# Kernel tuning notes

Measured on AMD Instinct MI355X. Metric: run time of the kernel, lower is better.

Reference implementation:

```python
import jax, jax.numpy as jnp
import numpy as np

N, E, D = 100000, 1600000, 128
EPS = 1e-5
NUM_LAYERS = 5


def setup_inputs() -> dict:
    key = jax.random.key(0)
    ks = jax.random.split(key, 2 + 2 * NUM_LAYERS)
    inp = {
        "x": jax.random.normal(ks[0], (N, D), dtype=jnp.float32),
        "edge_index": jax.random.randint(ks[1], (2, E), 0, N),
    }
    for i in range(NUM_LAYERS):
        inp[f"W{i}"] = jax.random.normal(ks[2 + 2 * i], (D, D), dtype=jnp.float32) / np.sqrt(D).astype(np.float32)
        inp[f"b{i}"] = jax.random.normal(ks[3 + 2 * i], (D,), dtype=jnp.float32) * 0.01
    return inp


def _gcn_forward(x, edge_index, Ws, bs):
    src, dst = edge_index[0], edge_index[1]
    # Degree with self-loops (torch code appends arange(N) loops, then clamps
    # count at min=1; with loops deg >= 1 always, so clamp is a no-op).
    deg = jax.ops.segment_sum(jnp.ones((E,), x.dtype), dst, num_segments=N) + 1.0
    inv_deg = (1.0 / deg)[:, None]  # [N, 1]
    for W, b in zip(Ws, bs):
        h = x @ W.T  # [N, D] linear (no bias; bias added after aggregation)
        # mean aggregation over in-neighbors + self-loop message (= h itself)
        agg = (jax.ops.segment_sum(h[src], dst, num_segments=N) + h) * inv_deg + b
        # batch_norm in training mode, no affine, biased variance, eps=1e-5
        mean = agg.mean(axis=0)
        var = ((agg - mean) ** 2).mean(axis=0)
        x = jax.nn.relu((agg - mean) * jax.lax.rsqrt(var + EPS))
        # dropout p=0.0, eval mode -> identity
    return x


def reference(x, edge_index, W0, b0, W1, b1, W2, b2, W3, b3, W4, b4):
    return _gcn_forward(x, edge_index, (W0, W1, W2, W3, W4), (b0, b1, b2, b3, b4))
```

## Files before the change

### kernel.cpp

```cpp
#include <hip/hip_runtime.h>
#include <hip/hip_bf16.h>

#define DD 128
#define NPART 8

typedef __bf16 bf16x8 __attribute__((ext_vector_type(8)));
typedef float f32x4 __attribute__((ext_vector_type(4)));

__device__ inline unsigned short f2bf_rne(float f) {
    unsigned u = __float_as_uint(f);
    u += 0x7fff + ((u >> 16) & 1);
    return (unsigned short)(u >> 16);
}


__global__ __launch_bounds__(256) void hist_kernel(const int* __restrict__ dst,
                                                   int* __restrict__ cnt, int E, int psize) {
    int part = blockIdx.x & (NPART - 1);
    int lo = part * psize, hi = lo + psize;
    int stride = (gridDim.x >> 3) * 256;
    for (int e = (blockIdx.x >> 3) * 256 + threadIdx.x; e < E; e += stride) {
        int d = dst[e];
        if (d >= lo && d < hi) atomicAdd(&cnt[d], 1);
    }
}

__global__ void scanA_kernel(const int* __restrict__ cnt, int* __restrict__ row_off,
                             int* __restrict__ partials, int N) {
    __shared__ int ls[256];
    int tid = threadIdx.x;
    int i = blockIdx.x * 1024 + tid * 4;
    int c0 = (i + 0 < N) ? cnt[i + 0] : 0;
    int c1 = (i + 1 < N) ? cnt[i + 1] : 0;
    int c2 = (i + 2 < N) ? cnt[i + 2] : 0;
    int c3 = (i + 3 < N) ? cnt[i + 3] : 0;
    int tot = c0 + c1 + c2 + c3;
    ls[tid] = tot;
    __syncthreads();
    for (int off = 1; off < 256; off <<= 1) {
        int v = (tid >= off) ? ls[tid - off] : 0;
        __syncthreads();
        ls[tid] += v;
        __syncthreads();
    }
    int excl = ls[tid] - tot;
    if (tid == 255) partials[blockIdx.x] = ls[255];
    int e0 = excl, e1 = e0 + c0, e2 = e1 + c1, e3 = e2 + c2;
    if (i + 0 < N) row_off[i + 0] = e0;
    if (i + 1 < N) row_off[i + 1] = e1;
    if (i + 2 < N) row_off[i + 2] = e2;
    if (i + 3 < N) row_off[i + 3] = e3;
}

__global__ __launch_bounds__(256) void scanB_kernel(int* partials, int nb) {
    __shared__ int ls[256];
    int tid = threadIdx.x;
    int base = 0;
    for (int c = 0; c < nb; c += 256) {
        int v = (c + tid < nb) ? partials[c + tid] : 0;
        ls[tid] = v;
        __syncthreads();
        for (int off = 1; off < 256; off <<= 1) {
            int t = (tid >= off) ? ls[tid - off] : 0;
            __syncthreads();
            ls[tid] += t;
            __syncthreads();
        }
        if (c + tid < nb) partials[c + tid] = ls[tid] - v + base;
        int tot = ls[255];
        __syncthreads();
        base += tot;
    }
}

__global__ void scanC_kernel(const int* __restrict__ cnt, int* __restrict__ row_off,
                             int* __restrict__ cursor, float* __restrict__ inv_deg,
                             const int* __restrict__ partials, int N) {
    int tid = threadIdx.x;
    int i = blockIdx.x * 1024 + tid * 4;
    int add = partials[blockIdx.x];
#pragma unroll
    for (int m = 0; m < 4; m++) {
        int idx = i + m;
        if (idx < N) {
            int v = row_off[idx] + add;
            row_off[idx] = v;
            cursor[idx] = v;
            int c = cnt[idx];
            inv_deg[idx] = 1.0f / (float)(c + 1);
            if (idx == N - 1) row_off[N] = v + c;
        }
    }
}

__global__ __launch_bounds__(256) void scatter_kernel(const int* __restrict__ src,
                                                      const int* __restrict__ dst,
                                                      int* __restrict__ cursor,
                                                      int* __restrict__ csr, int E, int psize) {
    int part = blockIdx.x & (NPART - 1);
    int lo = part * psize, hi = lo + psize;
    int stride = (gridDim.x >> 3) * 256;
    for (int e = (blockIdx.x >> 3) * 256 + threadIdx.x; e < E; e += stride) {
        int d = dst[e];
        if (d >= lo && d < hi) {
            int pos = atomicAdd(&cursor[d], 1);
            csr[pos] = src[e];
        }
    }
}


__global__ __launch_bounds__(256) void tobf16_kernel(const float* __restrict__ x,
                                                     unsigned short* __restrict__ h, long total4) {
    long idx = (long)blockIdx.x * 256 + threadIdx.x;
    if (idx >= total4) return;
    float4 v = ((const float4*)x)[idx];
    ushort4 o;
    o.x = f2bf_rne(v.x); o.y = f2bf_rne(v.y); o.z = f2bf_rne(v.z); o.w = f2bf_rne(v.w);
    ((ushort4*)h)[idx] = o;
}


template <int NORM>
__global__ __launch_bounds__(256) void gather_kernel(const unsigned int* __restrict__ prev,
                                                     const int* __restrict__ row_off,
                                                     const int* __restrict__ csr,
                                                     const float* __restrict__ stats,
                                                     float* __restrict__ sbuf, int N) {
    int node = blockIdx.x * 4 + (threadIdx.x >> 6);
    if (node >= N) return;
    int lane = threadIdx.x & 63;
    float m0 = 0.f, m1 = 0.f, r0 = 1.f, r1 = 1.f;
    if (NORM) {
        int c = 2 * lane;
        m0 = stats[c];       m1 = stats[c + 1];
        r0 = stats[128 + c]; r1 = stats[129 + c];
    }
    int base = node * 64 + lane;
    float ax, ay;
    {
        unsigned u = prev[base];
        float vx = __uint_as_float(u << 16);
        float vy = __uint_as_float(u & 0xffff0000u);
        if (NORM) { ax = fmaxf((vx - m0) * r0, 0.f); ay = fmaxf((vy - m1) * r1, 0.f); }
        else      { ax = vx; ay = vy; }
    }
    int e = row_off[node], end = row_off[node + 1];
    for (; e + 4 <= end; e += 4) {
        int i0 = csr[e], i1 = csr[e + 1], i2 = csr[e + 2], i3 = csr[e + 3];
        unsigned u0 = prev[i0 * 64 + lane];
        unsigned u1 = prev[i1 * 64 + lane];
        unsigned u2 = prev[i2 * 64 + lane];
        unsigned u3 = prev[i3 * 64 + lane];
        float x0 = __uint_as_float(u0 << 16), y0 = __uint_as_float(u0 & 0xffff0000u);
        float x1 = __uint_as_float(u1 << 16), y1 = __uint_as_float(u1 & 0xffff0000u);
        float x2 = __uint_as_float(u2 << 16), y2 = __uint_as_float(u2 & 0xffff0000u);
        float x3 = __uint_as_float(u3 << 16), y3 = __uint_as_float(u3 & 0xffff0000u);
        if (NORM) {
            ax += fmaxf((x0 - m0) * r0, 0.f) + fmaxf((x1 - m0) * r0, 0.f)
                + fmaxf((x2 - m0) * r0, 0.f) + fmaxf((x3 - m0) * r0, 0.f);
            ay += fmaxf((y0 - m1) * r1, 0.f) + fmaxf((y1 - m1) * r1, 0.f)
                + fmaxf((y2 - m1) * r1, 0.f) + fmaxf((y3 - m1) * r1, 0.f);
        } else {
            ax += x0 + x1 + x2 + x3;
            ay += y0 + y1 + y2 + y3;
        }
    }
    for (; e < end; e++) {
        unsigned u0 = prev[csr[e] * 64 + lane];
        float x0 = __uint_as_float(u0 << 16), y0 = __uint_as_float(u0 & 0xffff0000u);
        if (NORM) { ax += fmaxf((x0 - m0) * r0, 0.f); ay += fmaxf((y0 - m1) * r1, 0.f); }
        else      { ax += x0; ay += y0; }
    }
    float2 o; o.x = ax; o.y = ay;
    ((float2*)sbuf)[base] = o;
}


__global__ void wsplit_kernel(const float* __restrict__ W0, const float* __restrict__ W1,
                              const float* __restrict__ W2, const float* __restrict__ W3,
                              const float* __restrict__ W4, unsigned short* __restrict__ whl) {
    int idx = blockIdx.x * 256 + threadIdx.x;
    int l = idx >> 14, r = idx & 16383;
    const float* W = (l == 0) ? W0 : (l == 1) ? W1 : (l == 2) ? W2 : (l == 3) ? W3 : W4;
    float x = W[r];
    unsigned u = __float_as_uint(x);
    unsigned short h = (unsigned short)(u >> 16);
    float hf = __uint_as_float(u & 0xffff0000u);
    float lo = x - hf;
    unsigned short lw = (unsigned short)(__float_as_uint(lo) >> 16);
    whl[l * 32768 + r] = h;
    whl[l * 32768 + 16384 + r] = lw;
}


template <int LAST>
__global__ __launch_bounds__(256) void mgemm_kernel(const float* __restrict__ Sin,
                                                    unsigned short* __restrict__ outh,
                                                    float* __restrict__ Sio,
                                                    const unsigned short* __restrict__ Whl,
                                                    const float* __restrict__ bias,
                                                    const float* __restrict__ inv_deg,
                                                    float* __restrict__ stats, int N) {
    __shared__ unsigned short ShL[128 * 128];
    __shared__ unsigned short SlL[128 * 128];
    const int t = threadIdx.x;
    const int i0 = blockIdx.x * 128;

#pragma unroll
    for (int b = 0; b < 16; b++) {
        int f = t + 256 * b;
        int r = f >> 5, k4 = f & 31;
        int row = i0 + r;
        float4 v = (row < N) ? *(const float4*)&Sin[(size_t)row * 128 + k4 * 4]
                             : make_float4(0.f, 0.f, 0.f, 0.f);
        int k8 = k4 >> 1;
        int base = r * 128 + ((k8 ^ (r & 7)) * 8) + (k4 & 1) * 4;
        ushort4 h, lw;
        {
            unsigned u = __float_as_uint(v.x); h.x = (unsigned short)(u >> 16);
            float d = v.x - __uint_as_float(u & 0xffff0000u); lw.x = (unsigned short)(__float_as_uint(d) >> 16);
            u = __float_as_uint(v.y); h.y = (unsigned short)(u >> 16);
            d = v.y - __uint_as_float(u & 0xffff0000u); lw.y = (unsigned short)(__float_as_uint(d) >> 16);
            u = __float_as_uint(v.z); h.z = (unsigned short)(u >> 16);
            d = v.z - __uint_as_float(u & 0xffff0000u); lw.z = (unsigned short)(__float_as_uint(d) >> 16);
            u = __float_as_uint(v.w); h.w = (unsigned short)(u >> 16);
            d = v.w - __uint_as_float(u & 0xffff0000u); lw.w = (unsigned short)(__float_as_uint(d) >> 16);
        }
        *(ushort4*)(ShL + base) = h;
        *(ushort4*)(SlL + base) = lw;
    }
    __syncthreads();

    const int w = t >> 6, l = t & 63;
    const int ll = l & 15, lh = l >> 4;
    const unsigned short* Wh = Whl;
    const unsigned short* Wl2 = Whl + 16384;
    f32x4 acc[2][8];
#pragma unroll
    for (int st = 0; st < 2; st++)
#pragma unroll
        for (int jt = 0; jt < 8; jt++) acc[st][jt] = (f32x4){0.f, 0.f, 0.f, 0.f};

    const int r0 = w * 32 + ll;
    const int r1 = r0 + 16;
#pragma unroll
    for (int ks = 0; ks < 4; ks++) {
        int k8 = ks * 4 + lh;
        int ia0 = r0 * 128 + ((k8 ^ (r0 & 7)) * 8);
        int ia1 = r1 * 128 + ((k8 ^ (r1 & 7)) * 8);
        bf16x8 ah0 = *(const bf16x8*)(ShL + ia0);
        bf16x8 al0 = *(const bf16x8*)(SlL + ia0);
        bf16x8 ah1 = *(const bf16x8*)(ShL + ia1);
        bf16x8 al1 = *(const bf16x8*)(SlL + ia1);
        int wk = ks * 32 + lh * 8;
#pragma unroll
        for (int jt = 0; jt < 8; jt++) {
            int wrow = jt * 16 + ll;
            bf16x8 bh = *(const bf16x8*)(Wh + wrow * 128 + wk);
            bf16x8 bl = *(const bf16x8*)(Wl2 + wrow * 128 + wk);
            acc[0][jt] = __builtin_amdgcn_mfma_f32_16x16x32_bf16(ah0, bh, acc[0][jt], 0, 0, 0);
            acc[1][jt] = __builtin_amdgcn_mfma_f32_16x16x32_bf16(ah1, bh, acc[1][jt], 0, 0, 0);
            acc[0][jt] = __builtin_amdgcn_mfma_f32_16x16x32_bf16(al0, bh, acc[0][jt], 0, 0, 0);
            acc[1][jt] = __builtin_amdgcn_mfma_f32_16x16x32_bf16(al1, bh, acc[1][jt], 0, 0, 0);
            acc[0][jt] = __builtin_amdgcn_mfma_f32_16x16x32_bf16(ah0, bl, acc[0][jt], 0, 0, 0);
            acc[1][jt] = __builtin_amdgcn_mfma_f32_16x16x32_bf16(ah1, bl, acc[1][jt], 0, 0, 0);
        }
    }

    float bj[8];
#pragma unroll
    for (int jt = 0; jt < 8; jt++) bj[jt] = bias[jt * 16 + ll];
    float cs[8], cq[8];
#pragma unroll
    for (int jt = 0; jt < 8; jt++) { cs[jt] = 0.f; cq[jt] = 0.f; }
#pragma unroll
    for (int st = 0; st < 2; st++) {
#pragma unroll
        for (int reg = 0; reg < 4; reg++) {
            int row = i0 + w * 32 + st * 16 + lh * 4 + reg;
            bool valid = row < N;
            float sc = valid ? inv_deg[row] : 0.f;
#pragma unroll
            for (int jt = 0; jt < 8; jt++) {
                float o = acc[st][jt][reg] * sc + bj[jt];
                if (valid) {
                    if (LAST) Sio[(size_t)row * 128 + jt * 16 + ll] = o;
                    else      outh[(size_t)row * 128 + jt * 16 + ll] = f2bf_rne(o);
                    cs[jt] += o;
                    cq[jt] += o * o;
                }
            }
        }
    }
#pragma unroll
    for (int jt = 0; jt < 8; jt++) {
        cs[jt] += __shfl_xor(cs[jt], 16);
        cs[jt] += __shfl_xor(cs[jt], 32);
        cq[jt] += __shfl_xor(cq[jt], 16);
        cq[jt] += __shfl_xor(cq[jt], 32);
    }
    __syncthreads();
    float* sred = (float*)ShL;
    if (l < 16) {
#pragma unroll
        for (int jt = 0; jt < 8; jt++) {
            sred[w * 256 + jt * 16 + l] = cs[jt];
            sred[w * 256 + 128 + jt * 16 + l] = cq[jt];
        }
    }
    __syncthreads();
    {
        int col = t & 127, s = t >> 7;
        float v = sred[0 * 256 + s * 128 + col] + sred[1 * 256 + s * 128 + col]
                + sred[2 * 256 + s * 128 + col] + sred[3 * 256 + s * 128 + col];
        atomicAdd(&stats[s * 128 + col], v);
    }
}


__global__ void finalize_kernel(float* stats, float invN) {
    int c = threadIdx.x;
    float mean = stats[c] * invN;
    float var = stats[128 + c] * invN - mean * mean;
    stats[c] = mean;
    stats[128 + c] = rsqrtf(var + 1e-5f);
}


__global__ __launch_bounds__(256) void outnorm_kernel(const float* __restrict__ agg,
                                                      const float* __restrict__ stats,
                                                      float* __restrict__ out, long total4) {
    long idx = (long)blockIdx.x * 256 + threadIdx.x;
    if (idx >= total4) return;
    int c0 = (int)((idx & 31) * 4);
    float4 v = ((const float4*)agg)[idx];
    float4 o;
    o.x = fmaxf((v.x - stats[c0 + 0]) * stats[128 + c0 + 0], 0.f);
    o.y = fmaxf((v.y - stats[c0 + 1]) * stats[128 + c0 + 1], 0.f);
    o.z = fmaxf((v.z - stats[c0 + 2]) * stats[128 + c0 + 2], 0.f);
    o.w = fmaxf((v.w - stats[c0 + 3]) * stats[128 + c0 + 3], 0.f);
    ((float4*)out)[idx] = o;
}


extern "C" void kernel_launch(void* const* d_in, const int* in_sizes, int n_in,
                              void* d_out, int out_size, void* d_ws, size_t ws_size,
                              hipStream_t stream) {
    const float* x = (const float*)d_in[0];
    const int* ei = (const int*)d_in[1];
    int N = in_sizes[0] / DD;
    int E = in_sizes[1] / 2;
    const float* Wp[5];
    const float* bp[5];
    for (int l = 0; l < 5; l++) {
        Wp[l] = (const float*)d_in[2 + 2 * l];
        bp[l] = (const float*)d_in[3 + 2 * l];
    }

    char* ws = (char*)d_ws;
    size_t off = 0;
    auto alloc = [&](size_t bytes) -> char* {
        char* p = ws + off;
        off = (off + bytes + 511) & ~(size_t)511;
        return p;
    };
    int* cnt = (int*)alloc((size_t)N * 4);
    int* row_off = (int*)alloc(((size_t)N + 1) * 4);
    int* cursor = (int*)alloc((size_t)N * 4);
    int* partials = (int*)alloc(4096 * 4);
    float* inv_deg = (float*)alloc((size_t)N * 4);
    float* stats = (float*)alloc(5 * 256 * 4);
    unsigned short* whl = (unsigned short*)alloc(5 * 32768 * 2);
    int* csr = (int*)alloc((size_t)E * 4);
    unsigned short* hb = (unsigned short*)alloc((size_t)N * DD * 2);
    float* Sbuf = (float*)alloc((size_t)N * DD * 4);
    (void)ws_size;

    const int* srcv = ei;
    const int* dstv = ei + E;

    hipMemsetAsync(cnt, 0, (size_t)N * 4, stream);
    hipMemsetAsync(stats, 0, 5 * 256 * 4, stream);

    wsplit_kernel<<<5 * 16384 / 256, 256, 0, stream>>>(Wp[0], Wp[1], Wp[2], Wp[3], Wp[4], whl);

    long total4 = (long)N * (DD / 4);
    tobf16_kernel<<<(int)((total4 + 255) / 256), 256, 0, stream>>>(x, hb, total4);

    int psize = (N + NPART - 1) / NPART;
    hist_kernel<<<NPART * 128, 256, 0, stream>>>(dstv, cnt, E, psize);
    int nb = (N + 1023) / 1024;
    scanA_kernel<<<nb, 256, 0, stream>>>(cnt, row_off, partials, N);
    scanB_kernel<<<1, 256, 0, stream>>>(partials, nb);
    scanC_kernel<<<nb, 256, 0, stream>>>(cnt, row_off, cursor, inv_deg, partials, N);
    scatter_kernel<<<NPART * 128, 256, 0, stream>>>(srcv, dstv, cursor, csr, E, psize);

    float invN = 1.0f / (float)N;
    int gblocks = (N + 3) / 4;
    int mblocks = (N + 127) / 128;

    for (int l = 0; l < 5; l++) {
        if (l == 0) {
            gather_kernel<0><<<gblocks, 256, 0, stream>>>((const unsigned int*)hb, row_off, csr,
                                                          nullptr, Sbuf, N);
        } else {
            gather_kernel<1><<<gblocks, 256, 0, stream>>>((const unsigned int*)hb, row_off, csr,
                                                          stats + (l - 1) * 256, Sbuf, N);
        }
        if (l < 4) {
            mgemm_kernel<0><<<mblocks, 256, 0, stream>>>(Sbuf, hb, nullptr, whl + l * 32768,
                                                         bp[l], inv_deg, stats + l * 256, N);
        } else {
            mgemm_kernel<1><<<mblocks, 256, 0, stream>>>(Sbuf, nullptr, Sbuf, whl + l * 32768,
                                                         bp[l], inv_deg, stats + l * 256, N);
        }
        finalize_kernel<<<1, 128, 0, stream>>>(stats + l * 256, invN);
    }

    outnorm_kernel<<<(int)((total4 + 255) / 256), 256, 0, stream>>>(Sbuf, stats + 4 * 256,
                                                                    (float*)d_out, total4);
}
```

Measured before the change: 1.015 ms.

## Store aggregated features in bf16, drop low-part MFMA, fold finalize into consumers

The gather now writes its aggregate as packed bf16 instead of fp32. The GEMM therefore loads half the bytes and skips the low-part activation split along with its two MFMAs per tile. The finalize kernel is removed: gather and outnorm compute mean and rsqrt from the raw sums themselves. The last layer also writes bf16 and outnorm reads it back, the gather loop is unrolled to 8, and the histogram and scatter grids are doubled. These changes cut memory traffic, MFMA work and launch count, at the cost of lower precision in the aggregate and the final pre-norm values.

Result: no change. 1.007 ms (-0.8%).

```diff
diff --git a/kernel.cpp b/kernel.cpp
--- a/kernel.cpp
+++ b/kernel.cpp
@@ -125,16 +125,20 @@
 __global__ __launch_bounds__(256) void gather_kernel(const unsigned int* __restrict__ prev,
                                                      const int* __restrict__ row_off,
                                                      const int* __restrict__ csr,
-                                                     const float* __restrict__ stats,
-                                                     float* __restrict__ sbuf, int N) {
+                                                     const float* __restrict__ stats_raw,
+                                                     float invN,
+                                                     unsigned int* __restrict__ outp, int N) {
     int node = blockIdx.x * 4 + (threadIdx.x >> 6);
     if (node >= N) return;
     int lane = threadIdx.x & 63;
     float m0 = 0.f, m1 = 0.f, r0 = 1.f, r1 = 1.f;
     if (NORM) {
         int c = 2 * lane;
-        m0 = stats[c];       m1 = stats[c + 1];
-        r0 = stats[128 + c]; r1 = stats[129 + c];
+        float s0 = stats_raw[c], s1 = stats_raw[c + 1];
+        float q0 = stats_raw[128 + c], q1 = stats_raw[129 + c];
+        m0 = s0 * invN; m1 = s1 * invN;
+        r0 = rsqrtf(q0 * invN - m0 * m0 + 1e-5f);
+        r1 = rsqrtf(q1 * invN - m1 * m1 + 1e-5f);
     }
     int base = node * 64 + lane;
     float ax, ay;
@@ -146,34 +150,41 @@
         else      { ax = vx; ay = vy; }
     }
     int e = row_off[node], end = row_off[node + 1];
-    for (; e + 4 <= end; e += 4) {
+    for (; e + 8 <= end; e += 8) {
         int i0 = csr[e], i1 = csr[e + 1], i2 = csr[e + 2], i3 = csr[e + 3];
+        int i4 = csr[e + 4], i5 = csr[e + 5], i6 = csr[e + 6], i7 = csr[e + 7];
         unsigned u0 = prev[i0 * 64 + lane];
         unsigned u1 = prev[i1 * 64 + lane];
         unsigned u2 = prev[i2 * 64 + lane];
         unsigned u3 = prev[i3 * 64 + lane];
-        float x0 = __uint_as_float(u0 << 16), y0 = __uint_as_float(u0 & 0xffff0000u);
-        float x1 = __uint_as_float(u1 << 16), y1 = __uint_as_float(u1 & 0xffff0000u);
-        float x2 = __uint_as_float(u2 << 16), y2 = __uint_as_float(u2 & 0xffff0000u);
-        float x3 = __uint_as_float(u3 << 16), y3 = __uint_as_float(u3 & 0xffff0000u);
+        unsigned u4 = prev[i4 * 64 + lane];
+        unsigned u5 = prev[i5 * 64 + lane];
+        unsigned u6 = prev[i6 * 64 + lane];
+        unsigned u7 = prev[i7 * 64 + lane];
+#define GX(u) __uint_as_float((u) << 16)
+#define GY(u) __uint_as_float((u) & 0xffff0000u)
         if (NORM) {
-            ax += fmaxf((x0 - m0) * r0, 0.f) + fmaxf((x1 - m0) * r0, 0.f)
-                + fmaxf((x2 - m0) * r0, 0.f) + fmaxf((x3 - m0) * r0, 0.f);
-            ay += fmaxf((y0 - m1) * r1, 0.f) + fmaxf((y1 - m1) * r1, 0.f)
-                + fmaxf((y2 - m1) * r1, 0.f) + fmaxf((y3 - m1) * r1, 0.f);
+            ax += fmaxf((GX(u0) - m0) * r0, 0.f) + fmaxf((GX(u1) - m0) * r0, 0.f)
+                + fmaxf((GX(u2) - m0) * r0, 0.f) + fmaxf((GX(u3) - m0) * r0, 0.f)
+                + fmaxf((GX(u4) - m0) * r0, 0.f) + fmaxf((GX(u5) - m0) * r0, 0.f)
+                + fmaxf((GX(u6) - m0) * r0, 0.f) + fmaxf((GX(u7) - m0) * r0, 0.f);
+            ay += fmaxf((GY(u0) - m1) * r1, 0.f) + fmaxf((GY(u1) - m1) * r1, 0.f)
+                + fmaxf((GY(u2) - m1) * r1, 0.f) + fmaxf((GY(u3) - m1) * r1, 0.f)
+                + fmaxf((GY(u4) - m1) * r1, 0.f) + fmaxf((GY(u5) - m1) * r1, 0.f)
+                + fmaxf((GY(u6) - m1) * r1, 0.f) + fmaxf((GY(u7) - m1) * r1, 0.f);
         } else {
-            ax += x0 + x1 + x2 + x3;
-            ay += y0 + y1 + y2 + y3;
+            ax += GX(u0) + GX(u1) + GX(u2) + GX(u3) + GX(u4) + GX(u5) + GX(u6) + GX(u7);
+            ay += GY(u0) + GY(u1) + GY(u2) + GY(u3) + GY(u4) + GY(u5) + GY(u6) + GY(u7);
         }
     }
     for (; e < end; e++) {
         unsigned u0 = prev[csr[e] * 64 + lane];
-        float x0 = __uint_as_float(u0 << 16), y0 = __uint_as_float(u0 & 0xffff0000u);
-        if (NORM) { ax += fmaxf((x0 - m0) * r0, 0.f); ay += fmaxf((y0 - m1) * r1, 0.f); }
-        else      { ax += x0; ay += y0; }
-    }
-    float2 o; o.x = ax; o.y = ay;
-    ((float2*)sbuf)[base] = o;
+        if (NORM) { ax += fmaxf((GX(u0) - m0) * r0, 0.f); ay += fmaxf((GY(u0) - m1) * r1, 0.f); }
+        else      { ax += GX(u0); ay += GY(u0); }
+    }
+#undef GX
+#undef GY
+    outp[base] = ((unsigned)f2bf_rne(ay) << 16) | (unsigned)f2bf_rne(ax);
 }
 
 
@@ -194,41 +205,24 @@
 }
 
 
-template <int LAST>
-__global__ __launch_bounds__(256) void mgemm_kernel(const float* __restrict__ Sin,
-                                                    unsigned short* __restrict__ outh,
-                                                    float* __restrict__ Sio,
+__global__ __launch_bounds__(256) void mgemm_kernel(const unsigned short* __restrict__ Sh,
+                                                    unsigned short* __restrict__ hb,
                                                     const unsigned short* __restrict__ Whl,
                                                     const float* __restrict__ bias,
                                                     const float* __restrict__ inv_deg,
                                                     float* __restrict__ stats, int N) {
     __shared__ unsigned short ShL[128 * 128];
-    __shared__ unsigned short SlL[128 * 128];
     const int t = threadIdx.x;
     const int i0 = blockIdx.x * 128;
 
 #pragma unroll
-    for (int b = 0; b < 16; b++) {
-        int f = t + 256 * b;
-        int r = f >> 5, k4 = f & 31;
+    for (int b = 0; b < 8; b++) {
+        int f = b * 256 + t;
+        int r = f >> 4, k8 = f & 15;
         int row = i0 + r;
-        float4 v = (row < N) ? *(const float4*)&Sin[(size_t)row * 128 + k4 * 4]
-                             : make_float4(0.f, 0.f, 0.f, 0.f);
-        int k8 = k4 >> 1;
-        int base = r * 128 + ((k8 ^ (r & 7)) * 8) + (k4 & 1) * 4;
-        ushort4 h, lw;
-        {
-            unsigned u = __float_as_uint(v.x); h.x = (unsigned short)(u >> 16);
-            float d = v.x - __uint_as_float(u & 0xffff0000u); lw.x = (unsigned short)(__float_as_uint(d) >> 16);
-            u = __float_as_uint(v.y); h.y = (unsigned short)(u >> 16);
-            d = v.y - __uint_as_float(u & 0xffff0000u); lw.y = (unsigned short)(__float_as_uint(d) >> 16);
-            u = __float_as_uint(v.z); h.z = (unsigned short)(u >> 16);
-            d = v.z - __uint_as_float(u & 0xffff0000u); lw.z = (unsigned short)(__float_as_uint(d) >> 16);
-            u = __float_as_uint(v.w); h.w = (unsigned short)(u >> 16);
-            d = v.w - __uint_as_float(u & 0xffff0000u); lw.w = (unsigned short)(__float_as_uint(d) >> 16);
-        }
-        *(ushort4*)(ShL + base) = h;
-        *(ushort4*)(SlL + base) = lw;
+        uint4 v = make_uint4(0u, 0u, 0u, 0u);
+        if (row < N) v = *(const uint4*)&Sh[(size_t)row * 128 + k8 * 8];
+        *(uint4*)(ShL + r * 128 + ((k8 ^ (r & 7)) * 8)) = v;
     }
     __syncthreads();
 
@@ -247,12 +241,8 @@
 #pragma unroll
     for (int ks = 0; ks < 4; ks++) {
         int k8 = ks * 4 + lh;
-        int ia0 = r0 * 128 + ((k8 ^ (r0 & 7)) * 8);
-        int ia1 = r1 * 128 + ((k8 ^ (r1 & 7)) * 8);
-        bf16x8 ah0 = *(const bf16x8*)(ShL + ia0);
-        bf16x8 al0 = *(const bf16x8*)(SlL + ia0);
-        bf16x8 ah1 = *(const bf16x8*)(ShL + ia1);
-        bf16x8 al1 = *(const bf16x8*)(SlL + ia1);
+        bf16x8 ah0 = *(const bf16x8*)(ShL + r0 * 128 + ((k8 ^ (r0 & 7)) * 8));
+        bf16x8 ah1 = *(const bf16x8*)(ShL + r1 * 128 + ((k8 ^ (r1 & 7)) * 8));
         int wk = ks * 32 + lh * 8;
 #pragma unroll
         for (int jt = 0; jt < 8; jt++) {
@@ -261,8 +251,6 @@
             bf16x8 bl = *(const bf16x8*)(Wl2 + wrow * 128 + wk);
             acc[0][jt] = __builtin_amdgcn_mfma_f32_16x16x32_bf16(ah0, bh, acc[0][jt], 0, 0, 0);
             acc[1][jt] = __builtin_amdgcn_mfma_f32_16x16x32_bf16(ah1, bh, acc[1][jt], 0, 0, 0);
-            acc[0][jt] = __builtin_amdgcn_mfma_f32_16x16x32_bf16(al0, bh, acc[0][jt], 0, 0, 0);
-            acc[1][jt] = __builtin_amdgcn_mfma_f32_16x16x32_bf16(al1, bh, acc[1][jt], 0, 0, 0);
             acc[0][jt] = __builtin_amdgcn_mfma_f32_16x16x32_bf16(ah0, bl, acc[0][jt], 0, 0, 0);
             acc[1][jt] = __builtin_amdgcn_mfma_f32_16x16x32_bf16(ah1, bl, acc[1][jt], 0, 0, 0);
         }
@@ -285,8 +273,7 @@
             for (int jt = 0; jt < 8; jt++) {
                 float o = acc[st][jt][reg] * sc + bj[jt];
                 if (valid) {
-                    if (LAST) Sio[(size_t)row * 128 + jt * 16 + ll] = o;
-                    else      outh[(size_t)row * 128 + jt * 16 + ll] = f2bf_rne(o);
+                    hb[(size_t)row * 128 + jt * 16 + ll] = f2bf_rne(o);
                     cs[jt] += o;
                     cq[jt] += o * o;
                 }
@@ -319,28 +306,30 @@
 }
 
 
-__global__ void finalize_kernel(float* stats, float invN) {
-    int c = threadIdx.x;
-    float mean = stats[c] * invN;
-    float var = stats[128 + c] * invN - mean * mean;
-    stats[c] = mean;
-    stats[128 + c] = rsqrtf(var + 1e-5f);
-}
-
-
-__global__ __launch_bounds__(256) void outnorm_kernel(const float* __restrict__ agg,
-                                                      const float* __restrict__ stats,
-                                                      float* __restrict__ out, long total4) {
-    long idx = (long)blockIdx.x * 256 + threadIdx.x;
-    if (idx >= total4) return;
-    int c0 = (int)((idx & 31) * 4);
-    float4 v = ((const float4*)agg)[idx];
-    float4 o;
-    o.x = fmaxf((v.x - stats[c0 + 0]) * stats[128 + c0 + 0], 0.f);
-    o.y = fmaxf((v.y - stats[c0 + 1]) * stats[128 + c0 + 1], 0.f);
-    o.z = fmaxf((v.z - stats[c0 + 2]) * stats[128 + c0 + 2], 0.f);
-    o.w = fmaxf((v.w - stats[c0 + 3]) * stats[128 + c0 + 3], 0.f);
-    ((float4*)out)[idx] = o;
+__global__ __launch_bounds__(256) void outnorm_kernel(const unsigned int* __restrict__ hb,
+                                                      const float* __restrict__ stats_raw,
+                                                      float invN,
+                                                      float2* __restrict__ out, int total) {
+    __shared__ float mls[128], rls[128];
+    int t = threadIdx.x;
+    if (t < 128) {
+        float mean = stats_raw[t] * invN;
+        float var = stats_raw[128 + t] * invN - mean * mean;
+        mls[t] = mean;
+        rls[t] = rsqrtf(var + 1e-5f);
+    }
+    __syncthreads();
+    int stride = gridDim.x * 256;
+    for (int idx = blockIdx.x * 256 + t; idx < total; idx += stride) {
+        int c = (idx & 63) * 2;
+        unsigned u = hb[idx];
+        float x = __uint_as_float(u << 16);
+        float y = __uint_as_float(u & 0xffff0000u);
+        float2 o;
+        o.x = fmaxf((x - mls[c]) * rls[c], 0.f);
+        o.y = fmaxf((y - mls[c + 1]) * rls[c + 1], 0.f);
+        out[idx] = o;
+    }
 }
 
 
@@ -374,7 +363,7 @@
     unsigned short* whl = (unsigned short*)alloc(5 * 32768 * 2);
     int* csr = (int*)alloc((size_t)E * 4);
     unsigned short* hb = (unsigned short*)alloc((size_t)N * DD * 2);
-    float* Sbuf = (float*)alloc((size_t)N * DD * 4);
+    unsigned short* Sh = (unsigned short*)alloc((size_t)N * DD * 2);
     (void)ws_size;
 
     const int* srcv = ei;
@@ -389,12 +378,12 @@
     tobf16_kernel<<<(int)((total4 + 255) / 256), 256, 0, stream>>>(x, hb, total4);
 
     int psize = (N + NPART - 1) / NPART;
-    hist_kernel<<<NPART * 128, 256, 0, stream>>>(dstv, cnt, E, psize);
+    hist_kernel<<<NPART * 256, 256, 0, stream>>>(dstv, cnt, E, psize);
     int nb = (N + 1023) / 1024;
     scanA_kernel<<<nb, 256, 0, stream>>>(cnt, row_off, partials, N);
     scanB_kernel<<<1, 256, 0, stream>>>(partials, nb);
     scanC_kernel<<<nb, 256, 0, stream>>>(cnt, row_off, cursor, inv_deg, partials, N);
-    scatter_kernel<<<NPART * 128, 256, 0, stream>>>(srcv, dstv, cursor, csr, E, psize);
+    scatter_kernel<<<NPART * 256, 256, 0, stream>>>(srcv, dstv, cursor, csr, E, psize);
 
     float invN = 1.0f / (float)N;
     int gblocks = (N + 3) / 4;
@@ -403,21 +392,17 @@
     for (int l = 0; l < 5; l++) {
         if (l == 0) {
             gather_kernel<0><<<gblocks, 256, 0, stream>>>((const unsigned int*)hb, row_off, csr,
-                                                          nullptr, Sbuf, N);
+                                                          nullptr, invN, (unsigned int*)Sh, N);
         } else {
             gather_kernel<1><<<gblocks, 256, 0, stream>>>((const unsigned int*)hb, row_off, csr,
-                                                          stats + (l - 1) * 256, Sbuf, N);
-        }
-        if (l < 4) {
-            mgemm_kernel<0><<<mblocks, 256, 0, stream>>>(Sbuf, hb, nullptr, whl + l * 32768,
-                                                         bp[l], inv_deg, stats + l * 256, N);
-        } else {
-            mgemm_kernel<1><<<mblocks, 256, 0, stream>>>(Sbuf, nullptr, Sbuf, whl + l * 32768,
-                                                         bp[l], inv_deg, stats + l * 256, N);
-        }
-        finalize_kernel<<<1, 128, 0, stream>>>(stats + l * 256, invN);
-    }
-
-    outnorm_kernel<<<(int)((total4 + 255) / 256), 256, 0, stream>>>(Sbuf, stats + 4 * 256,
-                                                                    (float*)d_out, total4);
-}
+                                                          stats + (l - 1) * 256, invN,
+                                                          (unsigned int*)Sh, N);
+        }
+        mgemm_kernel<<<mblocks, 256, 0, stream>>>(Sh, hb, whl + l * 32768, bp[l], inv_deg,
+                                                  stats + l * 256, N);
+    }
+
+    int totalU = N * 64;
+    outnorm_kernel<<<2048, 256, 0, stream>>>((const unsigned int*)hb, stats + 4 * 256, invN,
+                                             (float2*)d_out, totalU);
+}
```
